# Performance work log

Hardware: AMD Instinct MI355X
Metric: run time of the kernel (lower is better)

## Reference

```python
import jax, jax.numpy as jnp
import numpy as np

B, L, D, H = 2, 2048, 1024, 16
NEG = -1.0e9


def setup_inputs() -> dict:
    key = jax.random.key(0)
    k1, k2, k3, k4 = jax.random.split(key, 4)
    query = jax.random.normal(k1, (B, L, D), dtype=jnp.float32)
    key_t = jax.random.normal(k2, (B, L, D), dtype=jnp.float32)
    value = jax.random.normal(k3, (B, L, D), dtype=jnp.float32)
    # Conv1D c_proj params: w ~ N(0, 0.02), b = 0   (nx=D -> nf=D)
    w_proj = 0.02 * jax.random.normal(k4, (D, D), dtype=jnp.float32)
    b_proj = jnp.zeros((D,), dtype=jnp.float32)
    return {"query": query, "key": key_t, "value": value,
            "w_proj": w_proj, "b_proj": b_proj, "n_head": H}


def reference(query, key, value, w_proj, b_proj, n_head):
    b, l, d = query.shape
    dh = d // n_head
    # split_heads -> [B, H, L, dh]
    q = query.reshape(b, l, n_head, dh).transpose(0, 2, 1, 3)
    k = key.reshape(b, l, n_head, dh).transpose(0, 2, 1, 3)
    v = value.reshape(b, l, n_head, dh).transpose(0, 2, 1, 3)
    # scores: [B, H, L, L], scaled by sqrt(head_dim) (v.size(-1) after split)
    w = jnp.einsum("bhqd,bhkd->bhqk", q, k) / jnp.sqrt(jnp.float32(dh))
    # one_dir_visible=True: multiplicative causal mask, w*m + (-1e9)*(1-m)
    m = jnp.tril(jnp.ones((l, l), dtype=w.dtype))[None, None]
    w = w * m + NEG * (1.0 - m)
    p = jax.nn.softmax(w, axis=-1)  # attn_dropout p=0 -> identity
    a = jnp.einsum("bhqk,bhkd->bhqd", p, v)  # [B, H, L, dh]
    # merge_heads -> [B, L, D]
    a = a.transpose(0, 2, 1, 3).reshape(b, l, d)
    # c_proj (Conv1D == dense): resid_dropout p=0 -> identity
    return a @ w_proj + b_proj
```

## Files before the change

kernel.cpp:

```cpp
#include <hip/hip_runtime.h>
#include <hip/hip_bf16.h>

constexpr int kB  = 2;
constexpr int kL  = 2048;
constexpr int kD  = 1024;
constexpr int kH  = 16;
constexpr int kDH = 64;
constexpr int kM  = kB * kL;

typedef _Float16 half8 __attribute__((ext_vector_type(8)));
typedef float    f32x4 __attribute__((ext_vector_type(4)));

constexpr size_t kKhOff = 0;
constexpr size_t kVtOff = 8388608;
constexpr size_t kAhOff = 16777216;
constexpr size_t kWtOff = 25165824;
constexpr size_t kWsNeed = 27262976;

__device__ __forceinline__ void load16_lds(const void* g, void* l) {
    __builtin_amdgcn_global_load_lds((__attribute__((address_space(1))) void*)(g),
                                     (__attribute__((address_space(3))) void*)(l),
                                     16, 0, 0);
}

__global__ __launch_bounds__(256) void conv_fused(const float* __restrict__ K,
                                                  const float* __restrict__ V,
                                                  const float* __restrict__ W,
                                                  _Float16* __restrict__ Kh,
                                                  _Float16* __restrict__ Vt,
                                                  _Float16* __restrict__ Wt) {
    const int t = threadIdx.x;
    const int bid = blockIdx.x;
    const int lane = t & 63, w = t >> 6;

    if (bid < 2048) {
        size_t i = ((size_t)bid * 256 + t) * 8;
        float4 f0 = *(const float4*)(K + i);
        float4 f1 = *(const float4*)(K + i + 4);
        half8 h;
        h[0] = (_Float16)f0.x; h[1] = (_Float16)f0.y; h[2] = (_Float16)f0.z; h[3] = (_Float16)f0.w;
        h[4] = (_Float16)f1.x; h[5] = (_Float16)f1.y; h[6] = (_Float16)f1.z; h[7] = (_Float16)f1.w;
        *(half8*)(Kh + i) = h;
    } else if (bid < 3072) {
        const int b2 = bid - 2048;
        const int lt = b2 & 31, h = (b2 >> 5) & 15, b = b2 >> 9;
        const float* src = V + (size_t)(b * kL + lt * 64) * kD + h * kDH + lane;
        _Float16* dst = Vt + ((size_t)(b * kH + h) * kDH + lane) * kL + lt * 64;
        #pragma unroll
        for (int g = 0; g < 2; ++g) {
            const int l0 = w * 16 + g * 8;
            half8 o;
            #pragma unroll
            for (int k = 0; k < 8; ++k)
                o[k] = (_Float16)src[(size_t)(l0 + k) * kD];
            *(half8*)(dst + l0) = o;
        }
    } else {
        const int b3 = bid - 3072;
        const int nt = b3 & 15, kt = b3 >> 4;
        const int k0 = kt * 64, n0 = nt * 64;
        const float* src = W + (size_t)k0 * kD + n0 + lane;
        _Float16* dst = Wt + (size_t)(n0 + lane) * kD + k0;
        #pragma unroll
        for (int g = 0; g < 2; ++g) {
            const int kk0 = w * 16 + g * 8;
            half8 o;
            #pragma unroll
            for (int k = 0; k < 8; ++k)
                o[k] = (_Float16)src[(size_t)(kk0 + k) * kD];
            *(half8*)(dst + kk0) = o;
        }
    }
}

__global__ __launch_bounds__(256, 4) void flash_kernel(const float* __restrict__ Q,
                                                       const _Float16* __restrict__ Kh,
                                                       const _Float16* __restrict__ Vt,
                                                       _Float16* __restrict__ Ah) {
    __shared__ __align__(16) _Float16 Ks[2][64 * 64];
    __shared__ __align__(16) _Float16 Vs[2][64 * 64];
    __shared__ __align__(16) _Float16 Ps[4][16 * 64];

    const int t = threadIdx.x;
    const int lane = t & 63, w = t >> 6;
    const int l15 = lane & 15, quad = lane >> 4;
    const int lhi = l15 >> 3, llo = l15 & 7;
    const int bid = blockIdx.x;
    const int bh = bid & 31;
    const int qt = 31 - (bid >> 5);
    const int b = bh >> 4, h = bh & 15;
    const int Tq = qt + 1;
    const int qrow0 = qt * 64 + w * 16;
    const size_t hoff = (size_t)h * kDH;

    const int srow = w * 16 + (lane >> 3);
    const int sj   = ((lane & 7) - (lane >> 3)) & 7;
    const _Float16* kgp = Kh + (size_t)(b * kL) * kD + hoff + sj * 8;
    const _Float16* vgp = Vt + (size_t)(bh * kDH) * kL + sj * 8;

    half8 aq[2];
    #pragma unroll
    for (int kc = 0; kc < 2; ++kc) {
        const float* qp = Q + (size_t)(b * kL + qrow0 + l15) * kD + hoff + kc * 32 + quad * 8;
        float4 f0 = *(const float4*)qp;
        float4 f1 = *(const float4*)(qp + 4);
        half8 hq;
        hq[0] = (_Float16)(f0.x * 0.125f); hq[1] = (_Float16)(f0.y * 0.125f);
        hq[2] = (_Float16)(f0.z * 0.125f); hq[3] = (_Float16)(f0.w * 0.125f);
        hq[4] = (_Float16)(f1.x * 0.125f); hq[5] = (_Float16)(f1.y * 0.125f);
        hq[6] = (_Float16)(f1.z * 0.125f); hq[7] = (_Float16)(f1.w * 0.125f);
        aq[kc] = hq;
    }

    half8 ones;
    #pragma unroll
    for (int i = 0; i < 8; ++i) ones[i] = (_Float16)1.0f;

    f32x4 o[4];
    f32x4 lsum = (f32x4){0.f, 0.f, 0.f, 0.f};
    #pragma unroll
    for (int nt = 0; nt < 4; ++nt) o[nt] = (f32x4){0.f, 0.f, 0.f, 0.f};

    _Float16* pp = Ps[w];

    constexpr float kLog2e = 1.4426950408889634f;
    constexpr float kBias  = -11.541560327111707f;

    load16_lds(kgp + (size_t)srow * kD,       &Ks[0][(w * 16) * 64]);
    load16_lds(kgp + (size_t)(srow + 8) * kD, &Ks[0][(w * 16 + 8) * 64]);
    load16_lds(vgp + (size_t)srow * kL,       &Vs[0][(w * 16) * 64]);
    load16_lds(vgp + (size_t)(srow + 8) * kL, &Vs[0][(w * 16 + 8) * 64]);

    for (int kt = 0; kt < Tq; ++kt) {
        const int cur = kt & 1;
        __syncthreads();

        if (kt + 1 < Tq) {
            const int kb1 = (kt + 1) * 64;
            load16_lds(kgp + (size_t)(kb1 + srow) * kD,     &Ks[cur ^ 1][(w * 16) * 64]);
            load16_lds(kgp + (size_t)(kb1 + srow + 8) * kD, &Ks[cur ^ 1][(w * 16 + 8) * 64]);
            load16_lds(vgp + (size_t)srow * kL + kb1,       &Vs[cur ^ 1][(w * 16) * 64]);
            load16_lds(vgp + (size_t)(srow + 8) * kL + kb1, &Vs[cur ^ 1][(w * 16 + 8) * 64]);
        }

        f32x4 s[4];
        #pragma unroll
        for (int nt = 0; nt < 4; ++nt) {
            s[nt] = (f32x4){0.f, 0.f, 0.f, 0.f};
            #pragma unroll
            for (int kc = 0; kc < 2; ++kc) {
                const int r = nt * 16 + l15;
                const int slot = (quad + 4 * kc + l15) & 7;
                half8 bk = *(half8*)&Ks[cur][r * 64 + slot * 8];
                s[nt] = __builtin_amdgcn_mfma_f32_16x16x32_f16(aq[kc], bk, s[nt], 0, 0, 0);
            }
        }

        if (kt == Tq - 1) {
            const int kb = kt * 64;
            const int row = qrow0 + quad * 4;
            #pragma unroll
            for (int nt = 0; nt < 4; ++nt)
                #pragma unroll
                for (int r = 0; r < 4; ++r)
                    if (kb + nt * 16 + l15 > row + r) s[nt][r] = -1.0e30f;
        }

        #pragma unroll
        for (int nt = 0; nt < 4; ++nt)
            #pragma unroll
            for (int r = 0; r < 4; ++r) {
                float p = exp2f(fmaf(s[nt][r], kLog2e, kBias));
                const int prow = quad * 4 + r;
                const int slot = (nt * 2 + lhi + prow) & 7;
                pp[prow * 64 + slot * 8 + llo] = (_Float16)p;
            }

        half8 ap[2];
        #pragma unroll
        for (int kc = 0; kc < 2; ++kc) {
            const int slot = (kc * 4 + quad + l15) & 7;
            ap[kc] = *(half8*)&pp[l15 * 64 + slot * 8];
        }

        #pragma unroll
        for (int nt = 0; nt < 4; ++nt)
            #pragma unroll
            for (int kc = 0; kc < 2; ++kc) {
                const int r = nt * 16 + l15;
                const int slot = (quad + 4 * kc + l15) & 7;
                half8 bv = *(half8*)&Vs[cur][r * 64 + slot * 8];
                o[nt] = __builtin_amdgcn_mfma_f32_16x16x32_f16(ap[kc], bv, o[nt], 0, 0, 0);
            }
        lsum = __builtin_amdgcn_mfma_f32_16x16x32_f16(ap[0], ones, lsum, 0, 0, 0);
        lsum = __builtin_amdgcn_mfma_f32_16x16x32_f16(ap[1], ones, lsum, 0, 0, 0);
    }

    const size_t orow = (size_t)(b * kL + qrow0 + quad * 4);
    #pragma unroll
    for (int r = 0; r < 4; ++r) {
        float inv = 1.0f / lsum[r];
        #pragma unroll
        for (int nt = 0; nt < 4; ++nt)
            Ah[(orow + r) * kD + hoff + nt * 16 + l15] = (_Float16)(o[nt][r] * inv);
    }
}

__global__ __launch_bounds__(256, 4) void proj_half(const _Float16* __restrict__ Ah,
                                                    const _Float16* __restrict__ Wt,
                                                    const float* __restrict__ bias,
                                                    float* __restrict__ out) {
    __shared__ __align__(16) _Float16 As[2][64 * 64];
    __shared__ __align__(16) _Float16 Bs[2][64 * 64];

    const int t = threadIdx.x;
    const int lane = t & 63, w = t >> 6;
    const int l15 = lane & 15, quad = lane >> 4;
    const int m0 = (blockIdx.x >> 4) * 64;
    const int n0 = (blockIdx.x & 15) * 64;

    const int srow = w * 16 + (lane >> 3);
    const int sj   = ((lane & 7) - (lane >> 3)) & 7;
    const _Float16* agp = Ah + (size_t)(m0 + srow) * kD + sj * 8;
    const _Float16* bgp = Wt + (size_t)(n0 + srow) * kD + sj * 8;

    f32x4 c[4];
    #pragma unroll
    for (int nt = 0; nt < 4; ++nt) c[nt] = (f32x4){0.f, 0.f, 0.f, 0.f};

    load16_lds(agp,                    &As[0][(w * 16) * 64]);
    load16_lds(agp + (size_t)8 * kD,   &As[0][(w * 16 + 8) * 64]);
    load16_lds(bgp,                    &Bs[0][(w * 16) * 64]);
    load16_lds(bgp + (size_t)8 * kD,   &Bs[0][(w * 16 + 8) * 64]);

    for (int kt = 0; kt < 16; ++kt) {
        const int cur = kt & 1;
        __syncthreads();

        if (kt + 1 < 16) {
            const int k1 = (kt + 1) * 64;
            load16_lds(agp + k1,                  &As[cur ^ 1][(w * 16) * 64]);
            load16_lds(agp + (size_t)8 * kD + k1, &As[cur ^ 1][(w * 16 + 8) * 64]);
            load16_lds(bgp + k1,                  &Bs[cur ^ 1][(w * 16) * 64]);
            load16_lds(bgp + (size_t)8 * kD + k1, &Bs[cur ^ 1][(w * 16 + 8) * 64]);
        }

        #pragma unroll
        for (int kc = 0; kc < 2; ++kc) {
            const int arow = w * 16 + l15;
            const int aslot = (kc * 4 + quad + l15) & 7;
            half8 a = *(half8*)&As[cur][arow * 64 + aslot * 8];
            #pragma unroll
            for (int nt = 0; nt < 4; ++nt) {
                const int brow = nt * 16 + l15;
                const int bslot = (kc * 4 + quad + l15) & 7;
                half8 bf = *(half8*)&Bs[cur][brow * 64 + bslot * 8];
                c[nt] = __builtin_amdgcn_mfma_f32_16x16x32_f16(a, bf, c[nt], 0, 0, 0);
            }
        }
    }

    #pragma unroll
    for (int nt = 0; nt < 4; ++nt) {
        const int n = n0 + nt * 16 + l15;
        const float bv = bias[n];
        const int mrow = m0 + w * 16 + quad * 4;
        #pragma unroll
        for (int r = 0; r < 4; ++r)
            out[(size_t)(mrow + r) * kD + n] = c[nt][r] + bv;
    }
}

__global__ __launch_bounds__(256) void attn_kernel_f32(const float* __restrict__ Q,
                                                       const float* __restrict__ K,
                                                       const float* __restrict__ V,
                                                       float* __restrict__ A) {
    const int lane = threadIdx.x & 63;
    const int wave = threadIdx.x >> 6;
    const int tilesPerBH = kL / 4;
    const int bh = blockIdx.x / tilesPerBH;
    const int tile = blockIdx.x % tilesPerBH;
    const int b = bh / kH, h = bh % kH;
    const int qi = tile * 4 + wave;
    const size_t base = (size_t)b * kL * kD + (size_t)h * kDH;
    const float* kptr = K + base;
    const float* vptr = V + base;
    const float qd = Q[base + (size_t)qi * kD + lane] * 0.125f;
    float m = -3.0e38f, l = 0.0f, acc = 0.0f;
    for (int j = 0; j <= qi; ++j) {
        const float kd = kptr[(size_t)j * kD + lane];
        float s = qd * kd;
        #pragma unroll
        for (int off = 32; off; off >>= 1) s += __shfl_xor(s, off);
        const float mnew = fmaxf(m, s);
        const float corr = __expf(m - mnew);
        const float p = __expf(s - mnew);
        const float vd = vptr[(size_t)j * kD + lane];
        l = l * corr + p;
        acc = acc * corr + p * vd;
        m = mnew;
    }
    A[base + (size_t)qi * kD + lane] = acc / l;
}

__global__ __launch_bounds__(256) void proj_kernel_f32(const float* __restrict__ A,
                                                       const float* __restrict__ W,
                                                       const float* __restrict__ bias,
                                                       float* __restrict__ out) {
    __shared__ __align__(16) float As[16][64];
    __shared__ __align__(16) float Ws[16][64];
    const int t = threadIdx.x;
    const int m0 = blockIdx.x * 64, n0 = blockIdx.y * 64;
    const int tx = t & 15, ty = t >> 4;
    const int arow = t >> 2, acol4 = (t & 3) * 4;
    const int wrow = t >> 4, wcol4 = (t & 15) * 4;
    float c[4][4] = {};
    for (int k0 = 0; k0 < kD; k0 += 16) {
        const float4 av = *(const float4*)(A + (size_t)(m0 + arow) * kD + k0 + acol4);
        const float4 wv = *(const float4*)(W + (size_t)(k0 + wrow) * kD + n0 + wcol4);
        __syncthreads();
        As[acol4 + 0][arow] = av.x;
        As[acol4 + 1][arow] = av.y;
        As[acol4 + 2][arow] = av.z;
        As[acol4 + 3][arow] = av.w;
        *(float4*)&Ws[wrow][wcol4] = wv;
        __syncthreads();
        #pragma unroll
        for (int kk = 0; kk < 16; ++kk) {
            const float4 a = *(const float4*)&As[kk][ty * 4];
            const float4 wv2 = *(const float4*)&Ws[kk][tx * 4];
            c[0][0] += a.x * wv2.x; c[0][1] += a.x * wv2.y; c[0][2] += a.x * wv2.z; c[0][3] += a.x * wv2.w;
            c[1][0] += a.y * wv2.x; c[1][1] += a.y * wv2.y; c[1][2] += a.y * wv2.z; c[1][3] += a.y * wv2.w;
            c[2][0] += a.z * wv2.x; c[2][1] += a.z * wv2.y; c[2][2] += a.z * wv2.z; c[2][3] += a.z * wv2.w;
            c[3][0] += a.w * wv2.x; c[3][1] += a.w * wv2.y; c[3][2] += a.w * wv2.z; c[3][3] += a.w * wv2.w;
        }
    }
    const float4 bv = *(const float4*)(bias + n0 + tx * 4);
    #pragma unroll
    for (int i = 0; i < 4; ++i) {
        float4 o;
        o.x = c[i][0] + bv.x; o.y = c[i][1] + bv.y; o.z = c[i][2] + bv.z; o.w = c[i][3] + bv.w;
        *(float4*)(out + (size_t)(m0 + ty * 4 + i) * kD + n0 + tx * 4) = o;
    }
}

extern "C" void kernel_launch(void* const* d_in, const int* in_sizes, int n_in,
                              void* d_out, int out_size, void* d_ws, size_t ws_size,
                              hipStream_t stream) {
    const float* Q    = (const float*)d_in[0];
    const float* K    = (const float*)d_in[1];
    const float* V    = (const float*)d_in[2];
    const float* W    = (const float*)d_in[3];
    const float* bias = (const float*)d_in[4];
    float* out = (float*)d_out;

    if (ws_size >= kWsNeed) {
        char* ws = (char*)d_ws;
        _Float16* Kh = (_Float16*)(ws + kKhOff);
        _Float16* Vt = (_Float16*)(ws + kVtOff);
        _Float16* Ah = (_Float16*)(ws + kAhOff);
        _Float16* Wt = (_Float16*)(ws + kWtOff);

        conv_fused<<<dim3(3328), 256, 0, stream>>>(K, V, W, Kh, Vt, Wt);
        flash_kernel<<<dim3(1024), 256, 0, stream>>>(Q, Kh, Vt, Ah);
        proj_half<<<dim3(1024), 256, 0, stream>>>(Ah, Wt, bias, out);
    } else {
        float* A = (float*)d_ws;
        attn_kernel_f32<<<dim3(kB * kH * (kL / 4)), 256, 0, stream>>>(Q, K, V, A);
        proj_kernel_f32<<<dim3(kM / 64, kD / 64), 256, 0, stream>>>(A, W, bias, out);
    }
}
```

Before: 160.9 us.

## Halve flash-attention KV tile to 32 keys and double occupancy target

The flash kernel now walks keys in 32-wide tiles instead of 64, so it needs twice as many iterations. LDS buffers for K, V and P shrink by half, and the launch bound moves from 4 to 8 blocks per CU, so more waves can hide latency. The swizzle patterns are reworked for the narrower rows, and the causal mask now runs on the last two sub-tiles. In exchange the kernel pays for more barriers and more loop overhead per key, and each barrier interval has less MFMA work to hide latency behind.

```diff
diff --git a/kernel.cpp b/kernel.cpp
--- a/kernel.cpp
+++ b/kernel.cpp
@@ -73,13 +73,13 @@
     }
 }
 
-__global__ __launch_bounds__(256, 4) void flash_kernel(const float* __restrict__ Q,
+__global__ __launch_bounds__(256, 8) void flash_kernel(const float* __restrict__ Q,
                                                        const _Float16* __restrict__ Kh,
                                                        const _Float16* __restrict__ Vt,
                                                        _Float16* __restrict__ Ah) {
-    __shared__ __align__(16) _Float16 Ks[2][64 * 64];
-    __shared__ __align__(16) _Float16 Vs[2][64 * 64];
-    __shared__ __align__(16) _Float16 Ps[4][16 * 64];
+    __shared__ __align__(16) _Float16 Ks[2][32 * 64];
+    __shared__ __align__(16) _Float16 Vs[2][64 * 32];
+    __shared__ __align__(16) _Float16 Ps[4][16 * 32];
 
     const int t = threadIdx.x;
     const int lane = t & 63, w = t >> 6;
@@ -89,14 +89,17 @@
     const int bh = bid & 31;
     const int qt = 31 - (bid >> 5);
     const int b = bh >> 4, h = bh & 15;
-    const int Tq = qt + 1;
+    const int Tq = 2 * qt + 2;
     const int qrow0 = qt * 64 + w * 16;
     const size_t hoff = (size_t)h * kDH;
 
-    const int srow = w * 16 + (lane >> 3);
-    const int sj   = ((lane & 7) - (lane >> 3)) & 7;
-    const _Float16* kgp = Kh + (size_t)(b * kL) * kD + hoff + sj * 8;
-    const _Float16* vgp = Vt + (size_t)(bh * kDH) * kL + sj * 8;
+    const int srowK = w * 8 + (lane >> 3);
+    const int sjK   = ((lane & 7) - (lane >> 3)) & 7;
+    const _Float16* kgp = Kh + (size_t)(b * kL) * kD + hoff + sjK * 8;
+
+    const int srowV = w * 16 + (lane >> 2);
+    const int sjV   = ((lane & 3) - (lane >> 2) - (lane >> 4)) & 3;
+    const _Float16* vgp = Vt + ((size_t)(bh * kDH) + srowV) * kL + sjV * 8;
 
     half8 aq[2];
     #pragma unroll
@@ -126,74 +129,63 @@
     constexpr float kLog2e = 1.4426950408889634f;
     constexpr float kBias  = -11.541560327111707f;
 
-    load16_lds(kgp + (size_t)srow * kD,       &Ks[0][(w * 16) * 64]);
-    load16_lds(kgp + (size_t)(srow + 8) * kD, &Ks[0][(w * 16 + 8) * 64]);
-    load16_lds(vgp + (size_t)srow * kL,       &Vs[0][(w * 16) * 64]);
-    load16_lds(vgp + (size_t)(srow + 8) * kL, &Vs[0][(w * 16 + 8) * 64]);
+    load16_lds(kgp + (size_t)srowK * kD, &Ks[0][(w * 8) * 64]);
+    load16_lds(vgp,                      &Vs[0][(w * 16) * 32]);
 
     for (int kt = 0; kt < Tq; ++kt) {
         const int cur = kt & 1;
         __syncthreads();
 
         if (kt + 1 < Tq) {
-            const int kb1 = (kt + 1) * 64;
-            load16_lds(kgp + (size_t)(kb1 + srow) * kD,     &Ks[cur ^ 1][(w * 16) * 64]);
-            load16_lds(kgp + (size_t)(kb1 + srow + 8) * kD, &Ks[cur ^ 1][(w * 16 + 8) * 64]);
-            load16_lds(vgp + (size_t)srow * kL + kb1,       &Vs[cur ^ 1][(w * 16) * 64]);
-            load16_lds(vgp + (size_t)(srow + 8) * kL + kb1, &Vs[cur ^ 1][(w * 16 + 8) * 64]);
-        }
-
-        f32x4 s[4];
-        #pragma unroll
-        for (int nt = 0; nt < 4; ++nt) {
+            const int kb1 = (kt + 1) * 32;
+            load16_lds(kgp + (size_t)(kb1 + srowK) * kD, &Ks[cur ^ 1][(w * 8) * 64]);
+            load16_lds(vgp + kb1,                        &Vs[cur ^ 1][(w * 16) * 32]);
+        }
+
+        f32x4 s[2];
+        #pragma unroll
+        for (int nt = 0; nt < 2; ++nt) {
             s[nt] = (f32x4){0.f, 0.f, 0.f, 0.f};
             #pragma unroll
             for (int kc = 0; kc < 2; ++kc) {
                 const int r = nt * 16 + l15;
-                const int slot = (quad + 4 * kc + l15) & 7;
+                const int slot = (quad + 4 * kc + r) & 7;
                 half8 bk = *(half8*)&Ks[cur][r * 64 + slot * 8];
                 s[nt] = __builtin_amdgcn_mfma_f32_16x16x32_f16(aq[kc], bk, s[nt], 0, 0, 0);
             }
         }
 
-        if (kt == Tq - 1) {
-            const int kb = kt * 64;
+        if (kt >= 2 * qt) {
+            const int kb = kt * 32;
             const int row = qrow0 + quad * 4;
             #pragma unroll
-            for (int nt = 0; nt < 4; ++nt)
+            for (int nt = 0; nt < 2; ++nt)
                 #pragma unroll
                 for (int r = 0; r < 4; ++r)
                     if (kb + nt * 16 + l15 > row + r) s[nt][r] = -1.0e30f;
         }
 
         #pragma unroll
-        for (int nt = 0; nt < 4; ++nt)
+        for (int nt = 0; nt < 2; ++nt)
             #pragma unroll
             for (int r = 0; r < 4; ++r) {
                 float p = exp2f(fmaf(s[nt][r], kLog2e, kBias));
                 const int prow = quad * 4 + r;
-                const int slot = (nt * 2 + lhi + prow) & 7;
-                pp[prow * 64 + slot * 8 + llo] = (_Float16)p;
+                const int slot = (nt * 2 + lhi + prow + quad) & 3;
+                pp[prow * 32 + slot * 8 + llo] = (_Float16)p;
             }
 
-        half8 ap[2];
-        #pragma unroll
-        for (int kc = 0; kc < 2; ++kc) {
-            const int slot = (kc * 4 + quad + l15) & 7;
-            ap[kc] = *(half8*)&pp[l15 * 64 + slot * 8];
-        }
-
-        #pragma unroll
-        for (int nt = 0; nt < 4; ++nt)
-            #pragma unroll
-            for (int kc = 0; kc < 2; ++kc) {
-                const int r = nt * 16 + l15;
-                const int slot = (quad + 4 * kc + l15) & 7;
-                half8 bv = *(half8*)&Vs[cur][r * 64 + slot * 8];
-                o[nt] = __builtin_amdgcn_mfma_f32_16x16x32_f16(ap[kc], bv, o[nt], 0, 0, 0);
-            }
-        lsum = __builtin_amdgcn_mfma_f32_16x16x32_f16(ap[0], ones, lsum, 0, 0, 0);
-        lsum = __builtin_amdgcn_mfma_f32_16x16x32_f16(ap[1], ones, lsum, 0, 0, 0);
+        const int apslot = (quad + l15 + (l15 >> 2)) & 3;
+        half8 ap = *(half8*)&pp[l15 * 32 + apslot * 8];
+
+        #pragma unroll
+        for (int nt = 0; nt < 4; ++nt) {
+            const int r = nt * 16 + l15;
+            const int slot = (quad + l15 + (l15 >> 2)) & 3;
+            half8 bv = *(half8*)&Vs[cur][r * 32 + slot * 8];
+            o[nt] = __builtin_amdgcn_mfma_f32_16x16x32_f16(ap, bv, o[nt], 0, 0, 0);
+        }
+        lsum = __builtin_amdgcn_mfma_f32_16x16x32_f16(ap, ones, lsum, 0, 0, 0);
     }
 
     const size_t orow = (size_t)(b * kL + qrow0 + quad * 4);
```

Measured after the change: 184.7 us. +14.8%, slower.
